# Optimization experiments

Hardware: AMD Instinct MI355X
Metric: run time of the kernel (lower is better)

## Reference

```python
import jax, jax.numpy as jnp
import numpy as np

B, T, STEPS = 4096, 56, 28
H, ANN, ENC, DEC = 126, 30, 20, 15
DIN = 1 + DEC + H  # decoder GRU input width = 142


def _gru_step(h, x, Wih, Whh, bih, bhh):
    # torch GRU cell math; Wih: [3H, in], Whh: [3H, H]
    gi = x @ Wih.T + bih
    gh = h @ Whh.T + bhh
    ir, iz, inn = jnp.split(gi, 3, axis=-1)
    hr, hz, hn = jnp.split(gh, 3, axis=-1)
    r = jax.nn.sigmoid(ir + hr)
    z = jax.nn.sigmoid(iz + hz)
    n = jnp.tanh(inn + r * hn)
    return (1.0 - z) * n + z * h


def setup_inputs() -> dict:
    key = jax.random.key(0)
    ks = jax.random.split(key, 23)
    p = lambda k, s: jax.random.normal(k, s, dtype=jnp.float32) * 0.08
    return {
        "ann_data": jax.random.normal(ks[0], (B, ANN), dtype=jnp.float32),
        "encoder_data": jax.random.normal(ks[1], (T, B, ENC), dtype=jnp.float32),
        "decoder_data": jax.random.normal(ks[2], (STEPS, B, DEC), dtype=jnp.float32),
        "s2h_W1": p(ks[3], (96, ANN)), "s2h_b1": p(ks[4], (96,)),
        "s2h_W2": p(ks[5], (H, 96)), "s2h_b2": p(ks[6], (H,)),
        "enc_Wih": p(ks[7], (3 * H, ENC)), "enc_Whh": p(ks[8], (3 * H, H)),
        "enc_bih": p(ks[9], (3 * H,)), "enc_bhh": p(ks[10], (3 * H,)),
        "dec_Wih": p(ks[11], (3 * H, DIN)), "dec_Whh": p(ks[12], (3 * H, H)),
        "dec_bih": p(ks[13], (3 * H,)), "dec_bhh": p(ks[14], (3 * H,)),
        "U_W": p(ks[15], (H, H)), "U_b": p(ks[16], (H,)),
        "Wl_W": p(ks[17], (H, H)), "Wl_b": p(ks[18], (H,)),
        "V_W": p(ks[19], (1, H)), "V_b": p(ks[20], (1,)),
        "h2o_W": p(ks[21], (1, H)), "h2o_b": p(ks[22], (1,)),
    }


def reference(ann_data, encoder_data, decoder_data,
              s2h_W1, s2h_b1, s2h_W2, s2h_b2,
              enc_Wih, enc_Whh, enc_bih, enc_bhh,
              dec_Wih, dec_Whh, dec_bih, dec_bhh,
              U_W, U_b, Wl_W, Wl_b, V_W, V_b, h2o_W, h2o_b):
    # static -> initial hidden: Linear(ANN,96) -> ReLU -> Linear(96,H)
    hidden = jnp.maximum(ann_data @ s2h_W1.T + s2h_b1, 0.0) @ s2h_W2.T + s2h_b2  # [B,H]

    def enc_f(h, x):
        h2 = _gru_step(h, x, enc_Wih, enc_Whh, enc_bih, enc_bhh)
        return h2, h2

    hidden, enc_out = jax.lax.scan(enc_f, hidden, encoder_data)  # enc_out: [T,B,H]

    Uo = enc_out @ U_W.T + U_b            # [T,B,H] precomputed (loop-invariant)
    gt0 = encoder_data[-1, :, 0:1]        # initial_ground, [B,1]

    def dec_f(carry, dec_x):
        h, prev = carry
        Wh = h @ Wl_W.T + Wl_b                              # [B,H]
        scores = jnp.tanh(Uo + Wh[None]) @ V_W.T + V_b      # [T,B,1]
        alpha = jax.nn.softmax(scores, axis=0)              # softmax over time
        attn = jnp.einsum('tb,tbh->bh', alpha[..., 0], enc_out)
        x = jnp.concatenate([prev, dec_x, attn], axis=1)    # [B,DIN]
        h2 = _gru_step(h, x, dec_Wih, dec_Whh, dec_bih, dec_bhh)
        out = h2 @ h2o_W.T + h2o_b                          # [B,1]
        return (h2, out), out

    _, outputs = jax.lax.scan(dec_f, (hidden, gt0), decoder_data)
    return outputs  # [STEPS, B, 1]
```

## Files before the change

### kernel.cpp

```cpp
#include <hip/hip_runtime.h>
#include <stdint.h>

typedef unsigned int u32;
typedef unsigned short u16;
typedef _Float16 f16;
typedef _Float16 f16x8 __attribute__((ext_vector_type(8)));
typedef _Float16 f16x4 __attribute__((ext_vector_type(4)));
typedef _Float16 f16x2 __attribute__((ext_vector_type(2)));
typedef float f32x4 __attribute__((ext_vector_type(4)));

constexpr int NB = 4096;
constexpr int NT = 56;
constexpr int NS = 28;
constexpr int NH = 126;
constexpr int NHP = 128;
constexpr float LOG2E = 1.4426950408889634f;

constexpr int LROW = 136;
constexpr int LB   = NT * LROW + 8;

constexpr size_t OFF_H    = 0;
constexpr size_t OFF_ENC  = 2097152;
constexpr size_t OFF_UO   = OFF_ENC + 58720256;
constexpr size_t OFF_WENC = OFF_UO + 58720256;
constexpr size_t OFF_WDEC = OFF_WENC + 122880;
constexpr size_t OFF_WL   = OFF_WDEC + 221184;
constexpr size_t OFF_UW   = OFF_WL + 32768;

__device__ __forceinline__ float fexp2(float x){ return __builtin_amdgcn_exp2f(x); }
__device__ __forceinline__ float frcp (float x){ return __builtin_amdgcn_rcpf(x); }
__device__ __forceinline__ float sigm (float x){ return frcp(1.f + fexp2(-LOG2E * x)); }
__device__ __forceinline__ float ftanh(float x){ return 1.f - 2.f * frcp(1.f + fexp2(2.f * LOG2E * x)); }
__device__ __forceinline__ float asf(u32 u){ union { u32 i; float f; } v; v.i = u; return v.f; }
__device__ __forceinline__ u16 tobf(float f){ union { float f; u32 i; } v; v.f = f;
  return (u16)((v.i + 0x7fffu + ((v.i >> 16) & 1u)) >> 16); }

__global__ void k_prep(const float* __restrict__ eWih, const float* __restrict__ eWhh,
                       const float* __restrict__ dWih, const float* __restrict__ dWhh,
                       const float* __restrict__ UW,   const float* __restrict__ Wl,
                       char* __restrict__ ws)
{
  f16* wenc = (f16*)(ws + OFF_WENC);
  f16* wdec = (f16*)(ws + OFF_WDEC);
  f16* wl   = (f16*)(ws + OFF_WL);
  f16* uw   = (f16*)(ws + OFF_UW);
  const int nE = 384 * 160, nD = 384 * 288, nW = 128 * 128;
  const int total = nE + nD + nW + nW;
  for (int i = blockIdx.x * 256 + threadIdx.x; i < total; i += gridDim.x * 256) {
    int idx = i;
    if (idx < nE) {
      const int r = idx / 160, c = idx % 160;
      float v = 0.f;
      if (r < 378) {
        if (c < 20) v = eWih[r * 20 + c];
        else if (c >= 32 && c < 158) v = eWhh[r * 126 + (c - 32)];
      }
      wenc[idx] = (f16)v; continue;
    }
    idx -= nE;
    if (idx < nD) {
      const int r = idx / 288, c = idx % 288;
      float v = 0.f;
      if (r < 378) {
        if (c < 16) v = dWih[r * 142 + c];
        else if (c >= 32 && c < 158) v = dWih[r * 142 + 16 + (c - 32)];
        else if (c >= 160 && c < 286) v = dWhh[r * 126 + (c - 160)];
      }
      wdec[idx] = (f16)v; continue;
    }
    idx -= nD;
    if (idx < nW) {
      const int r = idx >> 7, c = idx & 127;
      wl[idx] = (f16)((r < 126 && c < 126) ? Wl[r * 126 + c] : 0.f);
      continue;
    }
    idx -= nW;
    { const int r = idx >> 7, c = idx & 127;
      uw[idx] = (f16)((r < 126 && c < 126) ? UW[r * 126 + c] : 0.f); }
  }
}

__global__ __launch_bounds__(256) void k_mlp(
    const float* __restrict__ ann, const float* __restrict__ W1, const float* __restrict__ b1,
    const float* __restrict__ W2, const float* __restrict__ b2, float* __restrict__ hstate)
{
  __shared__ float anns[32][33];
  __shared__ float t1s[32][101];
  const int tid = threadIdx.x;
  const int b0 = blockIdx.x * 32;
  for (int i = tid; i < 32 * 30; i += 256)
    anns[i / 30][i % 30] = ann[(b0 + i / 30) * 30 + (i % 30)];
  __syncthreads();
  const int b = tid & 31, rg = tid >> 5;
  for (int m = rg; m < 96; m += 8) {
    float a = b1[m];
    for (int k = 0; k < 30; ++k) a += W1[m * 30 + k] * anns[b][k];
    t1s[b][m] = fmaxf(a, 0.f);
  }
  __syncthreads();
  for (int j = rg; j < NHP; j += 8) {
    float a = 0.f;
    if (j < NH) {
      a = b2[j];
      for (int k = 0; k < 96; ++k) a += W2[j * 96 + k] * t1s[b][k];
    }
    hstate[(b0 + b) * NHP + j] = a;
  }
}

__global__ __launch_bounds__(512) void k_enc(
    const float* __restrict__ xenc, const f16* __restrict__ Wenc,
    const f16* __restrict__ Uw,
    const float* __restrict__ bih, const float* __restrict__ bhh,
    const float* __restrict__ Ub,
    float* __restrict__ hstate, f16* __restrict__ encO, u16* __restrict__ uoO)
{
  __shared__ f16 av[16][296];
  const int tid = threadIdx.x;
  const int wid = tid >> 6, l = tid & 63, quad = l >> 4, col = l & 15;
  const int b0 = blockIdx.x * 16;
  const int jb = wid * 16, j = jb + col;
  const bool valid = j < NH;
  const int jc = valid ? j : NH - 1;

  const float br  = bih[jc]        + bhh[jc];
  const float bz  = bih[NH + jc]   + bhh[NH + jc];
  const float bnx = bih[2*NH + jc];
  const float bnh = bhh[2*NH + jc];
  const float ub  = Ub[jc];

  f16x8 rB[5], zB[5], nxB, nhB[4], uB[4];
  {
    const int ko = quad * 8, rr = jb + col;
#pragma unroll
    for (int kt = 0; kt < 5; ++kt) {
      rB[kt] = *(const f16x8*)&Wenc[rr * 160 + kt * 32 + ko];
      zB[kt] = *(const f16x8*)&Wenc[(NH + rr) * 160 + kt * 32 + ko];
    }
    nxB = *(const f16x8*)&Wenc[(2*NH + rr) * 160 + ko];
#pragma unroll
    for (int kt = 0; kt < 4; ++kt) {
      nhB[kt] = *(const f16x8*)&Wenc[(2*NH + rr) * 160 + 32 + kt * 32 + ko];
      uB[kt]  = *(const f16x8*)&Uw[rr * 128 + kt * 32 + ko];
    }
  }

  {
    const int bb = tid >> 5, c4 = (tid & 31) * 4;
    const float4 hv = *(const float4*)&hstate[(b0 + bb) * NHP + c4];
    av[bb][32 + c4]     = (f16)hv.x; av[bb][32 + c4 + 1] = (f16)hv.y;
    av[bb][32 + c4 + 2] = (f16)hv.z; av[bb][32 + c4 + 3] = (f16)hv.w;
  }
  if (tid < 192) { const int bb = tid / 12, p = tid % 12; av[bb][20 + p] = (f16)0.f; }
  __syncthreads();

  const int m = col, ko = quad * 8;
  for (int t = 0; t < NT; ++t) {
    const int hp = 32 + (t & 1) * 128, hq = 32 + ((t + 1) & 1) * 128;
    if (tid < 320) {
      const int bb = tid / 20, e = tid % 20;
      av[bb][e] = (f16)xenc[((size_t)t * NB + b0 + bb) * 20 + e];
    }
    __syncthreads();
    f16x8 A[5];
    A[0] = *(const f16x8*)&av[m][ko];
#pragma unroll
    for (int kt = 1; kt < 5; ++kt) A[kt] = *(const f16x8*)&av[m][hp + (kt - 1) * 32 + ko];

    f32x4 Cr = {br, br, br, br}, Cz = {bz, bz, bz, bz};
    f32x4 Cnx = {bnx, bnx, bnx, bnx}, Cnh = {bnh, bnh, bnh, bnh};
#pragma unroll
    for (int kt = 0; kt < 5; ++kt) {
      Cr = __builtin_amdgcn_mfma_f32_16x16x32_f16(A[kt], rB[kt], Cr, 0, 0, 0);
      Cz = __builtin_amdgcn_mfma_f32_16x16x32_f16(A[kt], zB[kt], Cz, 0, 0, 0);
    }
    Cnx = __builtin_amdgcn_mfma_f32_16x16x32_f16(A[0], nxB, Cnx, 0, 0, 0);
#pragma unroll
    for (int kt = 0; kt < 4; ++kt)
      Cnh = __builtin_amdgcn_mfma_f32_16x16x32_f16(A[kt + 1], nhB[kt], Cnh, 0, 0, 0);

    float hv4[4];
#pragma unroll
    for (int c = 0; c < 4; ++c) {
      const int bb = quad * 4 + c;
      const float hold = (float)av[bb][hp + j];
      const float r = sigm(Cr[c]), z = sigm(Cz[c]);
      const float n = ftanh(Cnx[c] + r * Cnh[c]);
      hv4[c] = (1.f - z) * n + z * hold;
    }
#pragma unroll
    for (int c = 0; c < 4; ++c) {
      const int bb = quad * 4 + c;
      const f16 hs = valid ? (f16)hv4[c] : (f16)0.f;
      av[bb][hq + j] = hs;
      encO[((size_t)(b0 + bb) * NT + t) * 128 + j] = hs;
    }
    if (t == NT - 1 && valid) {
#pragma unroll
      for (int c = 0; c < 4; ++c)
        hstate[(b0 + quad * 4 + c) * NHP + j] = hv4[c];
    }
    __syncthreads();

    f16x8 Ah[4];
#pragma unroll
    for (int kt = 0; kt < 4; ++kt) Ah[kt] = *(const f16x8*)&av[m][hq + kt * 32 + ko];
    f32x4 Cu = {ub, ub, ub, ub};
#pragma unroll
    for (int kt = 0; kt < 4; ++kt)
      Cu = __builtin_amdgcn_mfma_f32_16x16x32_f16(Ah[kt], uB[kt], Cu, 0, 0, 0);
#pragma unroll
    for (int c = 0; c < 4; ++c) {
      const u16 eu = tobf(fexp2(2.f * LOG2E * Cu[c]));
      uoO[((size_t)(b0 + quad * 4 + c) * NT + t) * 128 + j] = valid ? eu : (u16)0;
    }
  }
}

__global__ __launch_bounds__(512) void k_dec(
    const float* __restrict__ xdec, const float* __restrict__ xenc,
    const f16* __restrict__ Wdec, const f16* __restrict__ WlW,
    const float* __restrict__ bih, const float* __restrict__ bhh,
    const float* __restrict__ Wlb, const float* __restrict__ Vw,
    const float* __restrict__ Vb, const float* __restrict__ how,
    const float* __restrict__ hob, const float* __restrict__ hstate,
    const f16* __restrict__ encO, const u16* __restrict__ uoO,
    float* __restrict__ out)
{
  __shared__ __align__(16) u16 uoL[4 * LB];
  __shared__ __align__(16) f16 encL[4 * LB];
  __shared__ __align__(16) f16 av[5][424];
  __shared__ float EWS[4][132];
  __shared__ float scS[4][68];
  __shared__ __align__(16) f16 hows16[128];
  const int tid = threadIdx.x;
  const int wid = tid >> 6, l = tid & 63, quad = l >> 4, col = l & 15;
  const int b0 = blockIdx.x * 4;
  const int jb = wid * 16, j = jb + col;
  const bool valid = j < NH;
  const int jc = valid ? j : NH - 1;

  const float br  = bih[jc]        + bhh[jc];
  const float bz  = bih[NH + jc]   + bhh[NH + jc];
  const float bnx = bih[2*NH + jc];
  const float bnh = bhh[2*NH + jc];
  const float wb  = Wlb[jc];
  const float vb0 = Vb[0], hob0 = hob[0];

  f16x8 rB[9], zB[9], nxB[5], nhB[4], wlB[4];
  {
    const int ko = quad * 8, rr = jb + col;
#pragma unroll
    for (int kt = 0; kt < 9; ++kt) {
      rB[kt] = *(const f16x8*)&Wdec[rr * 288 + kt * 32 + ko];
      zB[kt] = *(const f16x8*)&Wdec[(NH + rr) * 288 + kt * 32 + ko];
    }
#pragma unroll
    for (int kt = 0; kt < 5; ++kt)
      nxB[kt] = *(const f16x8*)&Wdec[(2*NH + rr) * 288 + kt * 32 + ko];
#pragma unroll
    for (int kt = 0; kt < 4; ++kt) {
      nhB[kt] = *(const f16x8*)&Wdec[(2*NH + rr) * 288 + 160 + kt * 32 + ko];
      wlB[kt] = *(const f16x8*)&WlW[rr * 128 + kt * 32 + ko];
    }
  }

  const int g = tid >> 3, sub = tid & 7;
  float n2v[16], svsum = 0.f;
#pragma unroll
  for (int i = 0; i < 16; ++i) {
    const int jj = sub * 16 + i;
    const float v = (jj < NH) ? Vw[jj] : 0.f;
    n2v[i] = -2.f * v;
    svsum += v;
  }
  if (tid >= 256 && tid < 384) {
    const int q = tid - 256; hows16[q] = (f16)((q < NH) ? how[q] : 0.f);
  }
  for (int i = tid; i < 5 * 424; i += 512) av[i / 424][i % 424] = (f16)0.f;
  if (tid < 24) EWS[tid / 6][126 + tid % 6] = 0.f;
  {
    const size_t gb = (size_t)b0 * NT * 128;
    for (int i = tid; i < 4 * NT * 16; i += 512) {
      const int ch = i & 15, btr = i >> 4;
      const int bb = btr / NT, tt = btr % NT;
      const int dst = bb * LB + tt * LROW + ch * 8;
      const size_t src = gb + (size_t)btr * 128 + ch * 8;
      *(f16x8*)&uoL [dst] = *(const f16x8*)&uoO [src];
      *(f16x8*)&encL[dst] = *(const f16x8*)&encO[src];
    }
  }
  __syncthreads();
  if (tid < 128) {
    const int bb = tid >> 5, c4 = (tid & 31) * 4;
    const float4 hv = *(const float4*)&hstate[(b0 + bb) * NHP + c4];
    av[bb][160 + c4]     = (f16)hv.x; av[bb][160 + c4 + 1] = (f16)hv.y;
    av[bb][160 + c4 + 2] = (f16)hv.z; av[bb][160 + c4 + 3] = (f16)hv.w;
  }
  if (tid < 4) av[tid][0] = (f16)xenc[((size_t)(NT - 1) * NB + b0 + tid) * 20];
  __syncthreads();

  const int m = col, ko = quad * 8;
  const int arow = ((m & 3) == 0) ? (m >> 2) : 4;
  const int pb = tid & 3, pth = (tid >> 2) & 1, pjp = tid >> 3;

  for (int s = 0; s < NS; ++s) {
    const int hp = 160 + (s & 1) * 128, hq = 160 + ((s + 1) & 1) * 128;

    {
      f16x8 Ah[4];
#pragma unroll
      for (int kt = 0; kt < 4; ++kt) Ah[kt] = *(const f16x8*)&av[arow][hp + kt * 32 + ko];
      f32x4 Cw = {wb, wb, wb, wb};
#pragma unroll
      for (int kt = 0; kt < 4; ++kt)
        Cw = __builtin_amdgcn_mfma_f32_16x16x32_f16(Ah[kt], wlB[kt], Cw, 0, 0, 0);
      if (valid) EWS[quad][j] = fexp2(2.f * LOG2E * Cw[0]);
    }
    if (tid < 60) { const int bb = tid / 15, e = tid % 15;
      av[bb][1 + e] = (f16)xdec[((size_t)s * NB + b0 + bb) * 15 + e]; }
    __syncthreads();

    {
      const int sbb = g & 3, tb = g >> 2;
      float ew[16];
#pragma unroll
      for (int i = 0; i < 4; ++i)
        *(float4*)&ew[i * 4] = *(const float4*)&EWS[sbb][sub * 16 + i * 4];
      const u16* up0 = &uoL[sbb * LB + sub * 16];
      uint4 q0 = *(const uint4*)&up0[tb * LROW];
      uint4 q1 = *(const uint4*)&up0[tb * LROW + 8];
#pragma unroll
      for (int rd = 0; rd < 4; ++rd) {
        const int t = rd * 16 + tb;
        const u32 wsv[8] = {q0.x, q0.y, q0.z, q0.w, q1.x, q1.y, q1.z, q1.w};
        if (rd < 3) {
          const int tn = (t + 16 < NT) ? (t + 16) : (NT - 1);
          q0 = *(const uint4*)&up0[tn * LROW];
          q1 = *(const uint4*)&up0[tn * LROW + 8];
        }
        if (t < NT) {
          float ac0 = 0.f, ac1 = 0.f, ac2 = 0.f, ac3 = 0.f;
#pragma unroll
          for (int k = 0; k < 8; k += 2) {
            const float p0 = fmaf(asf(wsv[k]     << 16),          ew[2 * k],     1.f);
            const float p1 = fmaf(asf(wsv[k]     & 0xffff0000u),  ew[2 * k + 1], 1.f);
            const float p2 = fmaf(asf(wsv[k + 1] << 16),          ew[2 * k + 2], 1.f);
            const float p3 = fmaf(asf(wsv[k + 1] & 0xffff0000u),  ew[2 * k + 3], 1.f);
            ac0 = fmaf(n2v[2 * k],     frcp(p0), ac0);
            ac1 = fmaf(n2v[2 * k + 1], frcp(p1), ac1);
            ac2 = fmaf(n2v[2 * k + 2], frcp(p2), ac2);
            ac3 = fmaf(n2v[2 * k + 3], frcp(p3), ac3);
          }
          float acc = svsum + (ac0 + ac1) + (ac2 + ac3);
          acc += __shfl_xor(acc, 1, 64);
          acc += __shfl_xor(acc, 2, 64);
          acc += __shfl_xor(acc, 4, 64);
          if (sub == 0) scS[sbb][t] = fexp2(LOG2E * (acc + vb0));
        }
      }
    }
    __syncthreads();

    {
      const int j0 = pjp * 2;
      const f16* er = &encL[pb * LB + j0];
      const float* scp = &scS[pb][pth * 28];
      const int tbase = pth * 28;
      float Z0 = 0.f, Z1 = 0.f, a00 = 0.f, a01 = 0.f, a10 = 0.f, a11 = 0.f;
#pragma unroll
      for (int i2 = 0; i2 < 28; i2 += 2) {
        const float2 ev = *(const float2*)&scp[i2];
        const f16x2 v0 = *(const f16x2*)&er[(tbase + i2    ) * LROW];
        const f16x2 v1 = *(const f16x2*)&er[(tbase + i2 + 1) * LROW];
        Z0 += ev.x; Z1 += ev.y;
        a00 = fmaf(ev.x, (float)v0[0], a00);
        a01 = fmaf(ev.y, (float)v1[0], a01);
        a10 = fmaf(ev.x, (float)v0[1], a10);
        a11 = fmaf(ev.y, (float)v1[1], a11);
      }
      float Z = Z0 + Z1, a0 = a00 + a01, a1 = a10 + a11;
      a0 += __shfl_xor(a0, 4, 64);
      a1 += __shfl_xor(a1, 4, 64);
      Z  += __shfl_xor(Z, 4, 64);
      if (pth == 0) {
        const float inv = frcp(Z);
        f16x2 st; st[0] = (f16)(a0 * inv); st[1] = (f16)(a1 * inv);
        *(f16x2*)&av[pb][32 + j0] = st;
      }
    }
    __syncthreads();

    {
      f16x8 A[9];
#pragma unroll
      for (int kt = 0; kt < 5; ++kt) A[kt] = *(const f16x8*)&av[arow][kt * 32 + ko];
#pragma unroll
      for (int kt = 5; kt < 9; ++kt) A[kt] = *(const f16x8*)&av[arow][hp + (kt - 5) * 32 + ko];
      f32x4 Cr = {br, br, br, br}, Cz = {bz, bz, bz, bz};
      f32x4 Cnx = {bnx, bnx, bnx, bnx}, Cnh = {bnh, bnh, bnh, bnh};
#pragma unroll
      for (int kt = 0; kt < 9; ++kt) {
        Cr = __builtin_amdgcn_mfma_f32_16x16x32_f16(A[kt], rB[kt], Cr, 0, 0, 0);
        Cz = __builtin_amdgcn_mfma_f32_16x16x32_f16(A[kt], zB[kt], Cz, 0, 0, 0);
      }
#pragma unroll
      for (int kt = 0; kt < 5; ++kt)
        Cnx = __builtin_amdgcn_mfma_f32_16x16x32_f16(A[kt], nxB[kt], Cnx, 0, 0, 0);
#pragma unroll
      for (int kt = 0; kt < 4; ++kt)
        Cnh = __builtin_amdgcn_mfma_f32_16x16x32_f16(A[kt + 5], nhB[kt], Cnh, 0, 0, 0);
      {
        const float hold = (float)av[quad][hp + j];
        const float r = sigm(Cr[0]), z = sigm(Cz[0]);
        const float n = ftanh(Cnx[0] + r * Cnh[0]);
        const float h2 = (1.f - z) * n + z * hold;
        if (valid) av[quad][hq + j] = (f16)h2;
      }
    }
    __syncthreads();

    if (wid == 0) {
      f16x8 Ah2[4], hB[4];
      const f16x8 zz = {};
#pragma unroll
      for (int kt = 0; kt < 4; ++kt) {
        Ah2[kt] = *(const f16x8*)&av[arow][hq + kt * 32 + ko];
        hB[kt] = (col == 0) ? *(const f16x8*)&hows16[kt * 32 + ko] : zz;
      }
      f32x4 Co = {0.f, 0.f, 0.f, 0.f};
#pragma unroll
      for (int kt = 0; kt < 4; ++kt)
        Co = __builtin_amdgcn_mfma_f32_16x16x32_f16(Ah2[kt], hB[kt], Co, 0, 0, 0);
      if (col == 0) {
        const float o = Co[0] + hob0;
        out[(size_t)s * NB + b0 + quad] = o;
        av[quad][0] = (f16)o;
      }
    }
  }
}

extern "C" void kernel_launch(void* const* d_in, const int* in_sizes, int n_in,
                              void* d_out, int out_size, void* d_ws, size_t ws_size,
                              hipStream_t stream)
{
  const float* ann   = (const float*)d_in[0];
  const float* xenc  = (const float*)d_in[1];
  const float* xdec  = (const float*)d_in[2];
  const float* W1    = (const float*)d_in[3];
  const float* b1    = (const float*)d_in[4];
  const float* W2    = (const float*)d_in[5];
  const float* b2    = (const float*)d_in[6];
  const float* eWih  = (const float*)d_in[7];
  const float* eWhh  = (const float*)d_in[8];
  const float* ebih  = (const float*)d_in[9];
  const float* ebhh  = (const float*)d_in[10];
  const float* dWih  = (const float*)d_in[11];
  const float* dWhh  = (const float*)d_in[12];
  const float* dbih  = (const float*)d_in[13];
  const float* dbhh  = (const float*)d_in[14];
  const float* UW    = (const float*)d_in[15];
  const float* Ubias = (const float*)d_in[16];
  const float* Wl    = (const float*)d_in[17];
  const float* Wlb   = (const float*)d_in[18];
  const float* Vw    = (const float*)d_in[19];
  const float* Vb    = (const float*)d_in[20];
  const float* how   = (const float*)d_in[21];
  const float* hob   = (const float*)d_in[22];

  char* ws = (char*)d_ws;
  float* hstate = (float*)(ws + OFF_H);
  f16*   encB   = (f16*)(ws + OFF_ENC);
  u16*   uoB    = (u16*)(ws + OFF_UO);
  const f16* pWenc = (const f16*)(ws + OFF_WENC);
  const f16* pWdec = (const f16*)(ws + OFF_WDEC);
  const f16* pWl   = (const f16*)(ws + OFF_WL);
  const f16* pUW   = (const f16*)(ws + OFF_UW);

  k_prep<<<200, 256, 0, stream>>>(eWih, eWhh, dWih, dWhh, UW, Wl, ws);
  k_mlp <<<128, 256, 0, stream>>>(ann, W1, b1, W2, b2, hstate);
  k_enc <<<NB / 16, 512, 0, stream>>>(xenc, pWenc, pUW, ebih, ebhh, Ubias,
                                      hstate, encB, uoB);
  k_dec <<<NB / 4, 512, 0, stream>>>(xdec, xenc, pWdec, pWl, dbih, dbhh,
                                     Wlb, Vw, Vb, how, hob, hstate,
                                     encB, uoB, (float*)d_out);
}
```

Measured before the change: 603.4 us.

## Process eight batch rows per decoder block and stream Uo from global

Each decoder block now handles 8 batch rows instead of 4. This fills more MFMA rows (the 16-row tile previously used only 4 real rows) and halves the grid. The per-step Uo reads are moved out of LDS and streamed from global or L2 each step, leaving only the encoder outputs resident in LDS. It adds a launch-bounds occupancy hint of 2 blocks per CU, but global loads now sit inside the serial step loop and the register pressure may become tight.

```diff
diff --git a/kernel.cpp b/kernel.cpp
--- a/kernel.cpp
+++ b/kernel.cpp
@@ -217,7 +217,7 @@
   }
 }
 
-__global__ __launch_bounds__(512) void k_dec(
+__global__ __launch_bounds__(512, 2) void k_dec(
     const float* __restrict__ xdec, const float* __restrict__ xenc,
     const f16* __restrict__ Wdec, const f16* __restrict__ WlW,
     const float* __restrict__ bih, const float* __restrict__ bhh,
@@ -227,15 +227,14 @@
     const f16* __restrict__ encO, const u16* __restrict__ uoO,
     float* __restrict__ out)
 {
-  __shared__ __align__(16) u16 uoL[4 * LB];
-  __shared__ __align__(16) f16 encL[4 * LB];
-  __shared__ __align__(16) f16 av[5][424];
-  __shared__ float EWS[4][132];
-  __shared__ float scS[4][68];
+  __shared__ __align__(16) f16 encL[8 * LB];
+  __shared__ __align__(16) f16 av[9][424];
+  __shared__ float EWS[8][132];
+  __shared__ float scS[8][60];
   __shared__ __align__(16) f16 hows16[128];
   const int tid = threadIdx.x;
   const int wid = tid >> 6, l = tid & 63, quad = l >> 4, col = l & 15;
-  const int b0 = blockIdx.x * 4;
+  const int b0 = blockIdx.x * 8;
   const int jb = wid * 16, j = jb + col;
   const bool valid = j < NH;
   const int jc = valid ? j : NH - 1;
@@ -277,32 +276,32 @@
   if (tid >= 256 && tid < 384) {
     const int q = tid - 256; hows16[q] = (f16)((q < NH) ? how[q] : 0.f);
   }
-  for (int i = tid; i < 5 * 424; i += 512) av[i / 424][i % 424] = (f16)0.f;
-  if (tid < 24) EWS[tid / 6][126 + tid % 6] = 0.f;
+  for (int i = tid; i < 9 * 424; i += 512) av[i / 424][i % 424] = (f16)0.f;
+  if (tid < 48) EWS[tid / 6][126 + tid % 6] = 0.f;
   {
     const size_t gb = (size_t)b0 * NT * 128;
-    for (int i = tid; i < 4 * NT * 16; i += 512) {
+    for (int i = tid; i < 8 * NT * 16; i += 512) {
       const int ch = i & 15, btr = i >> 4;
       const int bb = btr / NT, tt = btr % NT;
-      const int dst = bb * LB + tt * LROW + ch * 8;
-      const size_t src = gb + (size_t)btr * 128 + ch * 8;
-      *(f16x8*)&uoL [dst] = *(const f16x8*)&uoO [src];
-      *(f16x8*)&encL[dst] = *(const f16x8*)&encO[src];
+      *(f16x8*)&encL[bb * LB + tt * LROW + ch * 8] =
+        *(const f16x8*)&encO[gb + (size_t)btr * 128 + ch * 8];
     }
   }
   __syncthreads();
-  if (tid < 128) {
+  if (tid < 256) {
     const int bb = tid >> 5, c4 = (tid & 31) * 4;
     const float4 hv = *(const float4*)&hstate[(b0 + bb) * NHP + c4];
     av[bb][160 + c4]     = (f16)hv.x; av[bb][160 + c4 + 1] = (f16)hv.y;
     av[bb][160 + c4 + 2] = (f16)hv.z; av[bb][160 + c4 + 3] = (f16)hv.w;
   }
-  if (tid < 4) av[tid][0] = (f16)xenc[((size_t)(NT - 1) * NB + b0 + tid) * 20];
+  if (tid < 8) av[tid][0] = (f16)xenc[((size_t)(NT - 1) * NB + b0 + tid) * 20];
   __syncthreads();
 
   const int m = col, ko = quad * 8;
-  const int arow = ((m & 3) == 0) ? (m >> 2) : 4;
-  const int pb = tid & 3, pth = (tid >> 2) & 1, pjp = tid >> 3;
+  const int arow = (m & 1) ? 8 : (m >> 1);
+  const int pb = tid & 7, pjp = tid >> 3;
+  const int p2b = g & 7, p2t = g >> 3;
+  const u16* eub = uoO + (size_t)(b0 + p2b) * NT * 128 + sub * 16;
 
   for (int s = 0; s < NS; ++s) {
     const int hp = 160 + (s & 1) * 128, hq = 160 + ((s + 1) & 1) * 128;
@@ -315,49 +314,47 @@
 #pragma unroll
       for (int kt = 0; kt < 4; ++kt)
         Cw = __builtin_amdgcn_mfma_f32_16x16x32_f16(Ah[kt], wlB[kt], Cw, 0, 0, 0);
-      if (valid) EWS[quad][j] = fexp2(2.f * LOG2E * Cw[0]);
-    }
-    if (tid < 60) { const int bb = tid / 15, e = tid % 15;
+      if (valid) {
+        EWS[2 * quad][j]     = fexp2(2.f * LOG2E * Cw[0]);
+        EWS[2 * quad + 1][j] = fexp2(2.f * LOG2E * Cw[2]);
+      }
+    }
+    if (tid < 120) { const int bb = tid / 15, e = tid % 15;
       av[bb][1 + e] = (f16)xdec[((size_t)s * NB + b0 + bb) * 15 + e]; }
     __syncthreads();
 
     {
-      const int sbb = g & 3, tb = g >> 2;
       float ew[16];
 #pragma unroll
       for (int i = 0; i < 4; ++i)
-        *(float4*)&ew[i * 4] = *(const float4*)&EWS[sbb][sub * 16 + i * 4];
-      const u16* up0 = &uoL[sbb * LB + sub * 16];
-      uint4 q0 = *(const uint4*)&up0[tb * LROW];
-      uint4 q1 = *(const uint4*)&up0[tb * LROW + 8];
-#pragma unroll
-      for (int rd = 0; rd < 4; ++rd) {
-        const int t = rd * 16 + tb;
+        *(float4*)&ew[i * 4] = *(const float4*)&EWS[p2b][sub * 16 + i * 4];
+      uint4 q0 = *(const uint4*)&eub[(size_t)p2t * 128];
+      uint4 q1 = *(const uint4*)&eub[(size_t)p2t * 128 + 8];
+#pragma unroll
+      for (int rd = 0; rd < 7; ++rd) {
+        const int t = rd * 8 + p2t;
         const u32 wsv[8] = {q0.x, q0.y, q0.z, q0.w, q1.x, q1.y, q1.z, q1.w};
-        if (rd < 3) {
-          const int tn = (t + 16 < NT) ? (t + 16) : (NT - 1);
-          q0 = *(const uint4*)&up0[tn * LROW];
-          q1 = *(const uint4*)&up0[tn * LROW + 8];
+        if (rd < 6) {
+          q0 = *(const uint4*)&eub[(size_t)(t + 8) * 128];
+          q1 = *(const uint4*)&eub[(size_t)(t + 8) * 128 + 8];
         }
-        if (t < NT) {
-          float ac0 = 0.f, ac1 = 0.f, ac2 = 0.f, ac3 = 0.f;
-#pragma unroll
-          for (int k = 0; k < 8; k += 2) {
-            const float p0 = fmaf(asf(wsv[k]     << 16),          ew[2 * k],     1.f);
-            const float p1 = fmaf(asf(wsv[k]     & 0xffff0000u),  ew[2 * k + 1], 1.f);
-            const float p2 = fmaf(asf(wsv[k + 1] << 16),          ew[2 * k + 2], 1.f);
-            const float p3 = fmaf(asf(wsv[k + 1] & 0xffff0000u),  ew[2 * k + 3], 1.f);
-            ac0 = fmaf(n2v[2 * k],     frcp(p0), ac0);
-            ac1 = fmaf(n2v[2 * k + 1], frcp(p1), ac1);
-            ac2 = fmaf(n2v[2 * k + 2], frcp(p2), ac2);
-            ac3 = fmaf(n2v[2 * k + 3], frcp(p3), ac3);
-          }
-          float acc = svsum + (ac0 + ac1) + (ac2 + ac3);
-          acc += __shfl_xor(acc, 1, 64);
-          acc += __shfl_xor(acc, 2, 64);
-          acc += __shfl_xor(acc, 4, 64);
-          if (sub == 0) scS[sbb][t] = fexp2(LOG2E * (acc + vb0));
+        float ac0 = 0.f, ac1 = 0.f, ac2 = 0.f, ac3 = 0.f;
+#pragma unroll
+        for (int k = 0; k < 8; k += 2) {
+          const float p0 = fmaf(asf(wsv[k]     << 16),          ew[2 * k],     1.f);
+          const float p1 = fmaf(asf(wsv[k]     & 0xffff0000u),  ew[2 * k + 1], 1.f);
+          const float p2 = fmaf(asf(wsv[k + 1] << 16),          ew[2 * k + 2], 1.f);
+          const float p3 = fmaf(asf(wsv[k + 1] & 0xffff0000u),  ew[2 * k + 3], 1.f);
+          ac0 = fmaf(n2v[2 * k],     frcp(p0), ac0);
+          ac1 = fmaf(n2v[2 * k + 1], frcp(p1), ac1);
+          ac2 = fmaf(n2v[2 * k + 2], frcp(p2), ac2);
+          ac3 = fmaf(n2v[2 * k + 3], frcp(p3), ac3);
         }
+        float acc = svsum + (ac0 + ac1) + (ac2 + ac3);
+        acc += __shfl_xor(acc, 1, 64);
+        acc += __shfl_xor(acc, 2, 64);
+        acc += __shfl_xor(acc, 4, 64);
+        if (sub == 0) scS[p2b][t] = fexp2(LOG2E * (acc + vb0));
       }
     }
     __syncthreads();
@@ -365,29 +362,33 @@
     {
       const int j0 = pjp * 2;
       const f16* er = &encL[pb * LB + j0];
-      const float* scp = &scS[pb][pth * 28];
-      const int tbase = pth * 28;
-      float Z0 = 0.f, Z1 = 0.f, a00 = 0.f, a01 = 0.f, a10 = 0.f, a11 = 0.f;
+      float Z0 = 0.f, Z1 = 0.f, Z2 = 0.f, Z3 = 0.f;
+      float a00 = 0.f, a01 = 0.f, a02 = 0.f, a03 = 0.f;
+      float a10 = 0.f, a11 = 0.f, a12 = 0.f, a13 = 0.f;
 #pragma unroll
       for (int i2 = 0; i2 < 28; i2 += 2) {
-        const float2 ev = *(const float2*)&scp[i2];
-        const f16x2 v0 = *(const f16x2*)&er[(tbase + i2    ) * LROW];
-        const f16x2 v1 = *(const f16x2*)&er[(tbase + i2 + 1) * LROW];
-        Z0 += ev.x; Z1 += ev.y;
-        a00 = fmaf(ev.x, (float)v0[0], a00);
-        a01 = fmaf(ev.y, (float)v1[0], a01);
-        a10 = fmaf(ev.x, (float)v0[1], a10);
-        a11 = fmaf(ev.y, (float)v1[1], a11);
-      }
-      float Z = Z0 + Z1, a0 = a00 + a01, a1 = a10 + a11;
-      a0 += __shfl_xor(a0, 4, 64);
-      a1 += __shfl_xor(a1, 4, 64);
-      Z  += __shfl_xor(Z, 4, 64);
-      if (pth == 0) {
-        const float inv = frcp(Z);
-        f16x2 st; st[0] = (f16)(a0 * inv); st[1] = (f16)(a1 * inv);
-        *(f16x2*)&av[pb][32 + j0] = st;
-      }
+        const float2 e01 = *(const float2*)&scS[pb][i2];
+        const float2 e23 = *(const float2*)&scS[pb][i2 + 28];
+        const f16x2 v0 = *(const f16x2*)&er[(i2     ) * LROW];
+        const f16x2 v1 = *(const f16x2*)&er[(i2 +  1) * LROW];
+        const f16x2 v2 = *(const f16x2*)&er[(i2 + 28) * LROW];
+        const f16x2 v3 = *(const f16x2*)&er[(i2 + 29) * LROW];
+        Z0 += e01.x; Z1 += e01.y; Z2 += e23.x; Z3 += e23.y;
+        a00 = fmaf(e01.x, (float)v0[0], a00);
+        a01 = fmaf(e01.y, (float)v1[0], a01);
+        a02 = fmaf(e23.x, (float)v2[0], a02);
+        a03 = fmaf(e23.y, (float)v3[0], a03);
+        a10 = fmaf(e01.x, (float)v0[1], a10);
+        a11 = fmaf(e01.y, (float)v1[1], a11);
+        a12 = fmaf(e23.x, (float)v2[1], a12);
+        a13 = fmaf(e23.y, (float)v3[1], a13);
+      }
+      const float Z  = (Z0 + Z1) + (Z2 + Z3);
+      const float a0 = (a00 + a01) + (a02 + a03);
+      const float a1 = (a10 + a11) + (a12 + a13);
+      const float inv = frcp(Z);
+      f16x2 st; st[0] = (f16)(a0 * inv); st[1] = (f16)(a1 * inv);
+      *(f16x2*)&av[pb][32 + j0] = st;
     }
     __syncthreads();
 
@@ -410,12 +411,14 @@
 #pragma unroll
       for (int kt = 0; kt < 4; ++kt)
         Cnh = __builtin_amdgcn_mfma_f32_16x16x32_f16(A[kt + 5], nhB[kt], Cnh, 0, 0, 0);
-      {
-        const float hold = (float)av[quad][hp + j];
-        const float r = sigm(Cr[0]), z = sigm(Cz[0]);
-        const float n = ftanh(Cnx[0] + r * Cnh[0]);
+#pragma unroll
+      for (int c = 0; c < 4; c += 2) {
+        const int bb = 2 * quad + (c >> 1);
+        const float hold = (float)av[bb][hp + j];
+        const float r = sigm(Cr[c]), z = sigm(Cz[c]);
+        const float n = ftanh(Cnx[c] + r * Cnh[c]);
         const float h2 = (1.f - z) * n + z * hold;
-        if (valid) av[quad][hq + j] = (f16)h2;
+        if (valid) av[bb][hq + j] = (f16)h2;
       }
     }
     __syncthreads();
@@ -433,9 +436,13 @@
       for (int kt = 0; kt < 4; ++kt)
         Co = __builtin_amdgcn_mfma_f32_16x16x32_f16(Ah2[kt], hB[kt], Co, 0, 0, 0);
       if (col == 0) {
-        const float o = Co[0] + hob0;
-        out[(size_t)s * NB + b0 + quad] = o;
-        av[quad][0] = (f16)o;
+#pragma unroll
+        for (int c = 0; c < 4; c += 2) {
+          const int bb = 2 * quad + (c >> 1);
+          const float o = Co[c] + hob0;
+          out[(size_t)s * NB + b0 + bb] = o;
+          av[bb][0] = (f16)o;
+        }
       }
     }
   }
@@ -482,7 +489,7 @@
   k_mlp <<<128, 256, 0, stream>>>(ann, W1, b1, W2, b2, hstate);
   k_enc <<<NB / 16, 512, 0, stream>>>(xenc, pWenc, pUW, ebih, ebhh, Ubias,
                                       hstate, encB, uoB);
-  k_dec <<<NB / 4, 512, 0, stream>>>(xdec, xenc, pWdec, pWl, dbih, dbhh,
+  k_dec <<<NB / 8, 512, 0, stream>>>(xdec, xenc, pWdec, pWl, dbih, dbhh,
                                      Wlb, Vw, Vb, how, hob, hstate,
                                      encB, uoB, (float*)d_out);
 }
```

Result: slower. 1.244 ms (+106.1%).
